# Optimization experiments

Hardware: AMD Instinct MI355X
Metric: run time of the kernel (lower is better)

Reference implementation:

```python
import jax, jax.numpy as jnp
import numpy as np

BIN_SIZE = 256
TOP_K = 16


def setup_inputs() -> dict:
    key = jax.random.key(0)
    kx, kc = jax.random.split(key)
    x = jax.random.normal(kx, (2, 4096, 512), dtype=jnp.float32)
    codebook = jax.random.normal(kc, (512, 16), dtype=jnp.float32)  # (feature_dim, max_num_bins//2)
    return {"x": x, "codebook": codebook}


def reference(x, codebook):
    B, N, F = x.shape
    n_bins = N // BIN_SIZE  # 16
    # LSH bucket assignment: project onto random hyperplanes, pick argmax of [p, -p]
    mul = x @ codebook[:, : n_bins // 2]                      # (B, N, n_bins//2)
    cmul = jnp.concatenate([mul, -mul], axis=-1)              # (B, N, n_bins)
    bin_idx = jnp.argmax(cmul, axis=-1)                       # (B, N)
    # argsort-based binning: equal-size bins of points sorted by bucket id
    bins_split = jnp.argsort(bin_idx, axis=-1).reshape(B, n_bins, BIN_SIZE)
    # gather points into bins: (B, n_bins, bin_size, F)
    points_binned = jnp.take_along_axis(x[:, None, :, :], bins_split[..., None], axis=2)
    # intra-bin dense similarity + sigmoid
    dm = jax.nn.sigmoid(jnp.einsum('bnif,bnjf->bnij', points_binned, points_binned))
    vals, idx = jax.lax.top_k(dm, TOP_K)                      # (B, n_bins, bin_size, k)
    # map local bin indices back to global point indices
    dst = jnp.take_along_axis(bins_split[:, :, None, :], idx, axis=-1)  # (B, nb, bs, k)
    src = jnp.broadcast_to(bins_split[..., None], dst.shape)
    b = jnp.broadcast_to(jnp.arange(B)[:, None, None, None], dst.shape)
    # dense equivalent of the coalesced batched sparse_coo_tensor of size (N, N)
    out = jnp.zeros((B, N, N), dtype=x.dtype).at[b, src, dst].add(vals)
    return out
```

## Files before the change

kernel.cpp:

```cpp
#include <hip/hip_runtime.h>
#include <stdint.h>
#include <math.h>

#define NPTS 4096
#define NF 512
#define NBINS 16
#define BSZ 256
#define TOPK 16
#define NBATCH 2
#define SPART (NBATCH * NBINS * BSZ * BSZ)

typedef float vf4 __attribute__((ext_vector_type(4)));

__global__ __launch_bounds__(256) void k_assign(const float* __restrict__ x,
                                                const float* __restrict__ cb,
                                                int* __restrict__ bin_idx) {
    int gw   = (blockIdx.x * 256 + threadIdx.x) >> 6;
    int lane = threadIdx.x & 63;
    const float* row = x + (size_t)gw * NF;
    float acc[8];
#pragma unroll
    for (int j = 0; j < 8; j++) acc[j] = 0.f;
    for (int f = lane; f < NF; f += 64) {
        float xv = row[f];
        const float4* c = (const float4*)(cb + f * 16);
        float4 c0 = c[0], c1 = c[1];
        acc[0] += xv * c0.x; acc[1] += xv * c0.y; acc[2] += xv * c0.z; acc[3] += xv * c0.w;
        acc[4] += xv * c1.x; acc[5] += xv * c1.y; acc[6] += xv * c1.z; acc[7] += xv * c1.w;
    }
#pragma unroll
    for (int off = 32; off > 0; off >>= 1) {
#pragma unroll
        for (int j = 0; j < 8; j++) acc[j] += __shfl_xor(acc[j], off, 64);
    }
    if (lane == 0) {
        float best = acc[0]; int bi = 0;
#pragma unroll
        for (int j = 1; j < 8; j++) { if (acc[j] > best) { best = acc[j]; bi = j; } }
#pragma unroll
        for (int j = 0; j < 8; j++) { float v = -acc[j]; if (v > best) { best = v; bi = 8 + j; } }
        bin_idx[gw] = bi;
    }
}

__global__ __launch_bounds__(256) void k_sort(const int* __restrict__ bin_idx,
                                              int* __restrict__ order) {
    __shared__ int s_eq[256];
    __shared__ int s_lt[256];
    int b   = blockIdx.x >> 4;
    int key = blockIdx.x & 15;
    int t   = threadIdx.x;
    const int* bi = bin_idx + b * NPTS;
    int base = t * 16;
    int e[16];
    { const int4* p = (const int4*)(bi + base);
      int4 a0 = p[0], a1 = p[1], a2 = p[2], a3 = p[3];
      e[0]=a0.x; e[1]=a0.y; e[2]=a0.z; e[3]=a0.w;
      e[4]=a1.x; e[5]=a1.y; e[6]=a1.z; e[7]=a1.w;
      e[8]=a2.x; e[9]=a2.y; e[10]=a2.z; e[11]=a2.w;
      e[12]=a3.x; e[13]=a3.y; e[14]=a3.z; e[15]=a3.w; }
    int ceq = 0, clt = 0;
#pragma unroll
    for (int i = 0; i < 16; i++) { ceq += (e[i] == key); clt += (e[i] < key); }
    s_eq[t] = ceq; s_lt[t] = clt;
    __syncthreads();
    int keybase = 0, myoff = 0;
    for (int u = 0; u < 256; u++) {
        keybase += s_lt[u];
        if (u < t) myoff += s_eq[u];
    }
    int* ob = order + b * NPTS + keybase;
#pragma unroll
    for (int i = 0; i < 16; i++) {
        if (e[i] == key) ob[myoff++] = base + i;
    }
}

__global__ __launch_bounds__(256, 2) void k_gemm(const float* __restrict__ x,
                                                 const int* __restrict__ order,
                                                 float* __restrict__ S) {
    int blk = blockIdx.x;
    int kh  = blk & 3;
    int tn  = (blk >> 2) & 1;
    int tm  = (blk >> 3) & 1;
    int bin = (blk >> 4) & 15;
    int b   = blk >> 8;
    int t  = threadIdx.x;
    int tx = t & 15, ty = t >> 4;
    __shared__ int   idxA[128];
    __shared__ int   idxB[128];
    __shared__ float Asl[32][132];
    __shared__ float Bsl[32][132];
    int ob = b * NPTS + bin * BSZ;
    if (t < 128) idxA[t] = order[ob + tm * 128 + t];
    else         idxB[t - 128] = order[ob + tn * 128 + (t - 128)];
    __syncthreads();
    const float* xb = x + (size_t)b * (NPTS * NF);
    int rowi = t & 127;
    int qb   = t >> 7;
    const float* rowA = xb + (size_t)idxA[rowi] * NF + kh * 128;
    const float* rowB = xb + (size_t)idxB[rowi] * NF + kh * 128;
    float acc[8][8];
#pragma unroll
    for (int i = 0; i < 8; i++)
#pragma unroll
        for (int j = 0; j < 8; j++) acc[i][j] = 0.f;
    float4 pa[4], pb[4];
#pragma unroll
    for (int l = 0; l < 4; l++) {
        pa[l] = *(const float4*)(rowA + (qb + 2 * l) * 4);
        pb[l] = *(const float4*)(rowB + (qb + 2 * l) * 4);
    }
    for (int it = 0; it < 4; it++) {
        __syncthreads();
#pragma unroll
        for (int l = 0; l < 4; l++) {
            int kq = (qb + 2 * l) * 4;
            Asl[kq + 0][rowi] = pa[l].x; Asl[kq + 1][rowi] = pa[l].y;
            Asl[kq + 2][rowi] = pa[l].z; Asl[kq + 3][rowi] = pa[l].w;
            Bsl[kq + 0][rowi] = pb[l].x; Bsl[kq + 1][rowi] = pb[l].y;
            Bsl[kq + 2][rowi] = pb[l].z; Bsl[kq + 3][rowi] = pb[l].w;
        }
        __syncthreads();
        if (it < 3) {
            const float* a2 = rowA + (it + 1) * 32;
            const float* b2 = rowB + (it + 1) * 32;
#pragma unroll
            for (int l = 0; l < 4; l++) {
                pa[l] = *(const float4*)(a2 + (qb + 2 * l) * 4);
                pb[l] = *(const float4*)(b2 + (qb + 2 * l) * 4);
            }
        }
#pragma unroll
        for (int kk = 0; kk < 32; kk++) {
            float4 a0 = *(const float4*)&Asl[kk][ty * 8];
            float4 a1 = *(const float4*)&Asl[kk][ty * 8 + 4];
            float4 b0 = *(const float4*)&Bsl[kk][tx * 8];
            float4 b1 = *(const float4*)&Bsl[kk][tx * 8 + 4];
            float av[8] = {a0.x, a0.y, a0.z, a0.w, a1.x, a1.y, a1.z, a1.w};
            float bv[8] = {b0.x, b0.y, b0.z, b0.w, b1.x, b1.y, b1.z, b1.w};
#pragma unroll
            for (int i = 0; i < 8; i++)
#pragma unroll
                for (int j = 0; j < 8; j++) acc[i][j] += av[i] * bv[j];
        }
    }
    float* Sp = S + (size_t)kh * SPART;
    size_t rowbase = (size_t)(b * NBINS + bin) * BSZ;
#pragma unroll
    for (int i = 0; i < 8; i++) {
        int r = tm * 128 + ty * 8 + i;
        float* orow = Sp + (rowbase + r) * BSZ + tn * 128 + tx * 8;
        *(float4*)(orow)     = make_float4(acc[i][0], acc[i][1], acc[i][2], acc[i][3]);
        *(float4*)(orow + 4) = make_float4(acc[i][4], acc[i][5], acc[i][6], acc[i][7]);
    }
}

__global__ __launch_bounds__(64) void k_topkw(const float* __restrict__ S,
                                              const int* __restrict__ order,
                                              float* __restrict__ out) {
    __shared__ float buf[NPTS];
    int row  = blockIdx.x;
    int lane = threadIdx.x;
    const float* s0 = S + (size_t)row * BSZ;
    vf4 v0 = *(const vf4*)&s0[4 * lane];
    vf4 v1 = *(const vf4*)&s0[4 * lane + SPART];
    vf4 v2 = *(const vf4*)&s0[4 * lane + 2 * SPART];
    vf4 v3 = *(const vf4*)&s0[4 * lane + 3 * SPART];
    unsigned long long key[4];
#pragma unroll
    for (int c = 0; c < 4; c++) {
        int j = 4 * lane + c;
        float d = v0[c] + v1[c] + v2[c] + v3[c];
        float v = 1.0f / (1.0f + expf(-d));
        key[c] = ((unsigned long long)__float_as_uint(v) << 32) | (unsigned)(255 - j);
    }
    int   wj[TOPK];
    float wv[TOPK];
#pragma unroll
    for (int it = 0; it < TOPK; it++) {
        unsigned long long k = key[0];
        if (key[1] > k) k = key[1];
        if (key[2] > k) k = key[2];
        if (key[3] > k) k = key[3];
#pragma unroll
        for (int off = 32; off > 0; off >>= 1) {
            unsigned long long o = __shfl_xor(k, off, 64);
            if (o > k) k = o;
        }
        int jw = 255 - (int)(k & 0xFFull);
        wj[it] = jw;
        wv[it] = __uint_as_float((unsigned)(k >> 32));
        if ((jw >> 2) == lane) {
            int c = jw & 3;
            if      (c == 0) key[0] = 0ull;
            else if (c == 1) key[1] = 0ull;
            else if (c == 2) key[2] = 0ull;
            else             key[3] = 0ull;
        }
    }
    vf4 z = {0.f, 0.f, 0.f, 0.f};
#pragma unroll
    for (int u = 0; u < 16; u++) ((vf4*)buf)[u * 64 + lane] = z;
    int b   = row >> 12;
    int bin = (row >> 8) & 15;
    int i   = row & 255;
    const int* obp = order + b * NPTS + bin * BSZ;
    int srcg = obp[i];
    __syncthreads();
#pragma unroll
    for (int it = 0; it < TOPK; it++) {
        if (lane == it) buf[obp[wj[it]]] = wv[it];
    }
    __syncthreads();
    vf4* orow = (vf4*)(out + ((size_t)b * NPTS + srcg) * NPTS);
#pragma unroll
    for (int u = 0; u < 16; u++) {
        __builtin_nontemporal_store(((const vf4*)buf)[u * 64 + lane], &orow[u * 64 + lane]);
    }
}

extern "C" void kernel_launch(void* const* d_in, const int* in_sizes, int n_in,
                              void* d_out, int out_size, void* d_ws, size_t ws_size,
                              hipStream_t stream) {
    const float* x  = (const float*)d_in[0];
    const float* cb = (const float*)d_in[1];
    float* out = (float*)d_out;
    int*   bin_idx = (int*)d_ws;
    int*   order   = bin_idx + NBATCH * NPTS;
    float* S       = (float*)d_ws + 4 * NBATCH * NPTS;

    k_assign<<<2048, 256, 0, stream>>>(x, cb, bin_idx);
    k_sort  <<<NBATCH * NBINS, 256, 0, stream>>>(bin_idx, order);
    k_gemm  <<<512, 256, 0, stream>>>(x, order, S);
    k_topkw <<<NBATCH * NPTS * NBINS / 16, 64, 0, stream>>>(S, order, out);
}
```

Baseline: 212.7 us.

## Widen gemm tile to full 256-column bin, halving blocks and A reloads

Each gemm block now computes a 128x256 tile (8x16 per thread) instead of 128x128, with the B tile covering the whole bin, so A rows are gathered once rather than twice. Thread-to-output mapping changes to strided 4-wide groups so LDS float4 reads spread across banks and global stores coalesce. The cost is a larger register footprint and more LDS, only 256 blocks on a large GPU (lower occupancy and parallelism), and the launch bound that requested 2 blocks per CU is dropped.

```diff
diff --git a/kernel.cpp b/kernel.cpp
--- a/kernel.cpp
+++ b/kernel.cpp
@@ -76,41 +76,39 @@
     }
 }
 
-__global__ __launch_bounds__(256, 2) void k_gemm(const float* __restrict__ x,
-                                                 const int* __restrict__ order,
-                                                 float* __restrict__ S) {
+__global__ __launch_bounds__(256) void k_gemm(const float* __restrict__ x,
+                                              const int* __restrict__ order,
+                                              float* __restrict__ S) {
     int blk = blockIdx.x;
     int kh  = blk & 3;
-    int tn  = (blk >> 2) & 1;
-    int tm  = (blk >> 3) & 1;
-    int bin = (blk >> 4) & 15;
-    int b   = blk >> 8;
+    int tm  = (blk >> 2) & 1;
+    int bin = (blk >> 3) & 15;
+    int b   = blk >> 7;
     int t  = threadIdx.x;
     int tx = t & 15, ty = t >> 4;
     __shared__ int   idxA[128];
-    __shared__ int   idxB[128];
+    __shared__ int   idxB[256];
     __shared__ float Asl[32][132];
-    __shared__ float Bsl[32][132];
+    __shared__ float Bsl[32][260];
     int ob = b * NPTS + bin * BSZ;
     if (t < 128) idxA[t] = order[ob + tm * 128 + t];
-    else         idxB[t - 128] = order[ob + tn * 128 + (t - 128)];
+    idxB[t] = order[ob + t];
     __syncthreads();
     const float* xb = x + (size_t)b * (NPTS * NF);
     int rowi = t & 127;
     int qb   = t >> 7;
     const float* rowA = xb + (size_t)idxA[rowi] * NF + kh * 128;
-    const float* rowB = xb + (size_t)idxB[rowi] * NF + kh * 128;
-    float acc[8][8];
+    const float* rowB = xb + (size_t)idxB[t]    * NF + kh * 128;
+    float acc[8][16];
 #pragma unroll
     for (int i = 0; i < 8; i++)
 #pragma unroll
-        for (int j = 0; j < 8; j++) acc[i][j] = 0.f;
-    float4 pa[4], pb[4];
-#pragma unroll
-    for (int l = 0; l < 4; l++) {
-        pa[l] = *(const float4*)(rowA + (qb + 2 * l) * 4);
-        pb[l] = *(const float4*)(rowB + (qb + 2 * l) * 4);
-    }
+        for (int j = 0; j < 16; j++) acc[i][j] = 0.f;
+    float4 pa[4], pb[8];
+#pragma unroll
+    for (int l = 0; l < 4; l++) pa[l] = *(const float4*)(rowA + (qb + 2 * l) * 4);
+#pragma unroll
+    for (int l = 0; l < 8; l++) pb[l] = *(const float4*)(rowB + l * 4);
     for (int it = 0; it < 4; it++) {
         __syncthreads();
 #pragma unroll
@@ -118,41 +116,49 @@
             int kq = (qb + 2 * l) * 4;
             Asl[kq + 0][rowi] = pa[l].x; Asl[kq + 1][rowi] = pa[l].y;
             Asl[kq + 2][rowi] = pa[l].z; Asl[kq + 3][rowi] = pa[l].w;
-            Bsl[kq + 0][rowi] = pb[l].x; Bsl[kq + 1][rowi] = pb[l].y;
-            Bsl[kq + 2][rowi] = pb[l].z; Bsl[kq + 3][rowi] = pb[l].w;
+        }
+#pragma unroll
+        for (int l = 0; l < 8; l++) {
+            Bsl[l * 4 + 0][t] = pb[l].x; Bsl[l * 4 + 1][t] = pb[l].y;
+            Bsl[l * 4 + 2][t] = pb[l].z; Bsl[l * 4 + 3][t] = pb[l].w;
         }
         __syncthreads();
         if (it < 3) {
             const float* a2 = rowA + (it + 1) * 32;
             const float* b2 = rowB + (it + 1) * 32;
 #pragma unroll
-            for (int l = 0; l < 4; l++) {
-                pa[l] = *(const float4*)(a2 + (qb + 2 * l) * 4);
-                pb[l] = *(const float4*)(b2 + (qb + 2 * l) * 4);
-            }
+            for (int l = 0; l < 4; l++) pa[l] = *(const float4*)(a2 + (qb + 2 * l) * 4);
+#pragma unroll
+            for (int l = 0; l < 8; l++) pb[l] = *(const float4*)(b2 + l * 4);
         }
 #pragma unroll
         for (int kk = 0; kk < 32; kk++) {
-            float4 a0 = *(const float4*)&Asl[kk][ty * 8];
-            float4 a1 = *(const float4*)&Asl[kk][ty * 8 + 4];
-            float4 b0 = *(const float4*)&Bsl[kk][tx * 8];
-            float4 b1 = *(const float4*)&Bsl[kk][tx * 8 + 4];
+            float4 a0 = *(const float4*)&Asl[kk][4 * ty];
+            float4 a1 = *(const float4*)&Asl[kk][4 * ty + 64];
+            float4 b0 = *(const float4*)&Bsl[kk][4 * tx];
+            float4 b1 = *(const float4*)&Bsl[kk][4 * tx + 64];
+            float4 b2 = *(const float4*)&Bsl[kk][4 * tx + 128];
+            float4 b3 = *(const float4*)&Bsl[kk][4 * tx + 192];
             float av[8] = {a0.x, a0.y, a0.z, a0.w, a1.x, a1.y, a1.z, a1.w};
-            float bv[8] = {b0.x, b0.y, b0.z, b0.w, b1.x, b1.y, b1.z, b1.w};
+            float bv[16] = {b0.x, b0.y, b0.z, b0.w, b1.x, b1.y, b1.z, b1.w,
+                            b2.x, b2.y, b2.z, b2.w, b3.x, b3.y, b3.z, b3.w};
 #pragma unroll
             for (int i = 0; i < 8; i++)
 #pragma unroll
-                for (int j = 0; j < 8; j++) acc[i][j] += av[i] * bv[j];
+                for (int j = 0; j < 16; j++) acc[i][j] += av[i] * bv[j];
         }
     }
     float* Sp = S + (size_t)kh * SPART;
-    size_t rowbase = (size_t)(b * NBINS + bin) * BSZ;
+    size_t rowbase = (size_t)(b * NBINS + bin) * BSZ + tm * 128;
 #pragma unroll
     for (int i = 0; i < 8; i++) {
-        int r = tm * 128 + ty * 8 + i;
-        float* orow = Sp + (rowbase + r) * BSZ + tn * 128 + tx * 8;
-        *(float4*)(orow)     = make_float4(acc[i][0], acc[i][1], acc[i][2], acc[i][3]);
-        *(float4*)(orow + 4) = make_float4(acc[i][4], acc[i][5], acc[i][6], acc[i][7]);
+        int r = 4 * ty + 64 * (i >> 2) + (i & 3);
+        float* orow = Sp + (rowbase + r) * BSZ;
+#pragma unroll
+        for (int g = 0; g < 4; g++) {
+            *(float4*)(orow + 4 * tx + 64 * g) =
+                make_float4(acc[i][4 * g], acc[i][4 * g + 1], acc[i][4 * g + 2], acc[i][4 * g + 3]);
+        }
     }
 }
 
@@ -232,6 +238,6 @@
 
     k_assign<<<2048, 256, 0, stream>>>(x, cb, bin_idx);
     k_sort  <<<NBATCH * NBINS, 256, 0, stream>>>(bin_idx, order);
-    k_gemm  <<<512, 256, 0, stream>>>(x, order, S);
+    k_gemm  <<<256, 256, 0, stream>>>(x, order, S);
     k_topkw <<<NBATCH * NPTS * NBINS / 16, 64, 0, stream>>>(S, order, out);
 }
```

After: 218.8 us. +2.9%, slower.
